# Performance work log

Measured on AMD Instinct MI355X. Metric: run time of the kernel, lower is better.

## Reference

```python
import jax, jax.numpy as jnp
import numpy as np

WORD, D, H = 512, 64, 8  # word_size, embed_dim (per-head), n_query

def setup_inputs() -> dict:
    key = jax.random.key(0)
    ks = jax.random.split(key, 9)
    B, S = 2, 4096
    sw = 1.0 / np.sqrt(WORD)
    x  = jax.random.normal(ks[0], (B, S, WORD), dtype=jnp.float32)
    Wk = jax.random.normal(ks[1], (WORD, D), dtype=jnp.float32) * sw
    bk = jnp.zeros((D,), jnp.float32)
    Wv = jax.random.normal(ks[2], (WORD, D), dtype=jnp.float32) * sw
    bv = jnp.zeros((D,), jnp.float32)
    Wq = jax.random.normal(ks[3], (H, WORD, D), dtype=jnp.float32) * sw
    bq = jnp.zeros((H, D), jnp.float32)
    Wp = jax.random.normal(ks[4], (H * D, D), dtype=jnp.float32) * (1.0 / np.sqrt(H * D))
    bp = jnp.zeros((D,), jnp.float32)
    return {"x": x, "Wq": Wq, "bq": bq, "Wk": Wk, "bk": bk, "Wv": Wv, "bv": bv, "Wp": Wp, "bp": bp}

def reference(x, Wq, bq, Wk, bk, Wv, bv, Wp, bp):
    # shared K/V across all query heads (multi-query attention)
    K = x @ Wk + bk                                   # [b, s, d]
    V = x @ Wv + bv                                   # [b, s, d]
    Q = jnp.einsum('bsw,hwd->bhsd', x, Wq) + bq[None, :, None, :]  # [b, h, s, d]
    scale = 1.0 / jnp.sqrt(jnp.float32(D))
    scores = jnp.einsum('bhsd,btd->bhst', Q, K) * scale  # [b, h, s, t]
    attn = jax.nn.softmax(scores, axis=-1)
    Z = jnp.einsum('bhst,btd->bhsd', attn, V)            # [b, h, s, d]
    B, _, S, _ = Z.shape
    Zc = jnp.transpose(Z, (0, 2, 1, 3)).reshape(B, S, H * D)  # concat heads
    return Zc @ Wp + bp                                   # [b, s, d]
```

## Files before the change

### kernel.cpp

```cpp
#include <hip/hip_runtime.h>
#include <hip/hip_bf16.h>
#include <stdint.h>

#define BB 2
#define SS 4096
#define WW 512
#define DD 64
#define HH 8
#define QSCALE 0.1803368801111244f

typedef __hip_bfloat16 bf16;
typedef __bf16 bf16x8 __attribute__((ext_vector_type(8)));
typedef float f32x16 __attribute__((ext_vector_type(16)));
typedef unsigned int u32x4 __attribute__((ext_vector_type(4)));
typedef unsigned int u32x2 __attribute__((ext_vector_type(2)));

union U4 { u32x4 u4; unsigned int u[4]; bf16x8 v; };

__device__ __forceinline__ float ldv(const float* p, size_t i) { return p[i]; }
__device__ __forceinline__ float ldv(const bf16* p, size_t i)  { return __bfloat162float(p[i]); }

__device__ __forceinline__ unsigned short f2bu(float f) {
    union Ub { bf16 b; unsigned short u; } t;
    t.b = __float2bfloat16(f);
    return t.u;
}

__device__ __forceinline__ float fast_exp2(float x) {
#if __has_builtin(__builtin_amdgcn_exp2f)
    return __builtin_amdgcn_exp2f(x);
#else
    return exp2f(x);
#endif
}

__device__ __forceinline__ f32x16 mfma_bf16(bf16x8 a, bf16x8 b, f32x16 c) {
    return __builtin_amdgcn_mfma_f32_32x32x16_bf16(a, b, c, 0, 0, 0);
}

__device__ __forceinline__ unsigned int pk_bf16(float lo, float hi) {
    unsigned int a = __float_as_uint(lo) + 0x8000u;
    unsigned int b = __float_as_uint(hi) + 0x8000u;
    return __builtin_amdgcn_perm(b, a, 0x07060302u);
}

__device__ __forceinline__ int block_detect(const void* raw, int* cntLds)
{
    if (threadIdx.x == 0) *cntLds = 0;
    __syncthreads();
    const bf16* xb = (const bf16*)raw;
    const float v = __bfloat162float(xb[2 * threadIdx.x]);
    const float a = fabsf(v);
    const bool insane = !(v == v) || (a >= 1.0e4f) || (a != 0.0f && a <= 1.0e-8f);
    const unsigned long long m = __ballot(insane);
    if ((threadIdx.x & 63) == 0) atomicAdd(cntLds, __popcll(m));
    __syncthreads();
    return (*cntLds * 2 > 256) ? 1 : 0;
}

template<typename T>
__device__ __forceinline__ void prep_w_body(
    const T* Wq, const T* bq, const T* Wk, const T* bk,
    const T* Wv, const T* bv, const T* Wp, const T* bp,
    unsigned short* Wb, float* bb, float (*Tt)[65], int pwblk)
{
    const int tid = threadIdx.x;
    const int cg = pwblk >> 3, wg = pwblk & 7;
    const int c0 = cg * 64, w0 = wg * 64;
    const T* src = (cg == 0) ? Wk : (cg == 1) ? Wv
                 : (cg == 10) ? Wp : (Wq + (size_t)(cg - 2) * WW * DD);
    const float scale = (cg >= 2 && cg < 10) ? QSCALE : 1.0f;

    #pragma unroll
    for (int i = 0; i < 16; ++i) {
        const int e = i * 256 + tid, w = e >> 6, d = e & 63;
        Tt[w][d] = ldv(src, (size_t)(w0 + w) * DD + d) * scale;
    }
    __syncthreads();
    #pragma unroll
    for (int i = 0; i < 16; ++i) {
        const int e = i * 256 + tid, d = e >> 6, w = e & 63;
        Wb[(size_t)(c0 + d) * WW + w0 + w] = f2bu(Tt[w][d]);
    }
    if (pwblk == 0) {
        #pragma unroll
        for (int i = 0; i < 3; ++i) {
            const int c = tid + i * 256;
            if (c < 704) {
                float v;
                if (c < 64)       v = ldv(bk, c);
                else if (c < 128) v = ldv(bv, c - 64);
                else if (c < 640) v = ldv(bq, c - 128) * QSCALE;
                else              v = ldv(bp, c - 640);
                bb[c] = v;
            }
        }
    }
}

__global__ __launch_bounds__(256) void prep_kernel(
    const void* x, const void* Wq, const void* bq, const void* Wk, const void* bk,
    const void* Wv, const void* bv, const void* Wp, const void* bp,
    unsigned short* xb, unsigned short* Wb, float* bb, int* flag)
{
    __shared__ float Tt[64][65];
    __shared__ int cnt;
    const int blk = blockIdx.x;

    if (blk < 2048) {
        const int fl = block_detect(x, &cnt);
        if (blk == 0 && threadIdx.x == 0) *flag = fl;
        const size_t i = ((size_t)blk * 256 + threadIdx.x) * 8;
        if (fl) {
            const float4* p = (const float4*)((const float*)x + i);
            const float4 a = p[0], b = p[1];
            unsigned int w[4];
            w[0] = pk_bf16(a.x, a.y); w[1] = pk_bf16(a.z, a.w);
            w[2] = pk_bf16(b.x, b.y); w[3] = pk_bf16(b.z, b.w);
            *(u32x4*)(xb + i) = *(u32x4*)w;
        } else {
            *(u32x4*)(xb + i) = *(const u32x4*)((const unsigned short*)x + i);
        }
    } else {
        const int fl = block_detect(Wk, &cnt);
        if (fl)
            prep_w_body<float>((const float*)Wq, (const float*)bq, (const float*)Wk,
                               (const float*)bk, (const float*)Wv, (const float*)bv,
                               (const float*)Wp, (const float*)bp, Wb, bb, Tt, blk - 2048);
        else
            prep_w_body<bf16>((const bf16*)Wq, (const bf16*)bq, (const bf16*)Wk,
                              (const bf16*)bk, (const bf16*)Wv, (const bf16*)bv,
                              (const bf16*)Wp, (const bf16*)bp, Wb, bb, Tt, blk - 2048);
    }
}

#define KP 40

__global__ __launch_bounds__(256, 2) void proj_mfma_kernel(
    const unsigned short* __restrict__ xb, const unsigned short* __restrict__ Wb,
    const float* __restrict__ bb,
    bf16* __restrict__ Kb, bf16* __restrict__ Vb, bf16* __restrict__ Qb)
{
    __shared__ unsigned short As[2][128 * KP];
    __shared__ unsigned short Bs[2][128 * KP];

    const int tid = threadIdx.x;
    const int wv = tid >> 6, ln = tid & 63;
    const int g = ln >> 5, cc = ln & 31;
    const int nblk = blockIdx.x % 5, mblk = blockIdx.x / 5;
    const int row0 = mblk * 128, n0 = nblk * 128;
    const int wm = (wv & 1) * 64, wn = (wv >> 1) * 64;

    const int sm = tid >> 2;
    const int sko = (tid & 3) * 8;

    u32x4 pa[2], pb[2];
    #define GLOAD(kt)                                                          \
        do {                                                                   \
            _Pragma("unroll")                                                  \
            for (int i = 0; i < 2; ++i) {                                      \
                const int m = sm + i * 64;                                     \
                pa[i] = *(const u32x4*)&xb[(size_t)(row0 + m) * WW + (kt) * 32 + sko]; \
                pb[i] = *(const u32x4*)&Wb[(size_t)(n0 + m) * WW + (kt) * 32 + sko];   \
            }                                                                  \
        } while (0)
    #define LWRITE(buf)                                                        \
        do {                                                                   \
            _Pragma("unroll")                                                  \
            for (int i = 0; i < 2; ++i) {                                      \
                const int m = sm + i * 64;                                     \
                *(u32x4*)&As[buf][m * KP + sko] = pa[i];                       \
                *(u32x4*)&Bs[buf][m * KP + sko] = pb[i];                       \
            }                                                                  \
        } while (0)

    f32x16 acc[2][2];
    #pragma unroll
    for (int a = 0; a < 2; ++a)
        #pragma unroll
        for (int c2 = 0; c2 < 2; ++c2)
            #pragma unroll
            for (int i = 0; i < 16; ++i) acc[a][c2][i] = 0.f;

    GLOAD(0); LWRITE(0);
    GLOAD(1);

    for (int kt = 0; kt < 16; ++kt) {
        __syncthreads();
        const int buf = kt & 1;
        #pragma unroll
        for (int ks = 0; ks < 2; ++ks) {
            U4 af[2], bfr[2];
            #pragma unroll
            for (int ms = 0; ms < 2; ++ms)
                af[ms].u4 = *(const u32x4*)&As[buf][(wm + ms * 32 + cc) * KP + ks * 16 + g * 8];
            #pragma unroll
            for (int ns = 0; ns < 2; ++ns)
                bfr[ns].u4 = *(const u32x4*)&Bs[buf][(wn + ns * 32 + cc) * KP + ks * 16 + g * 8];
            #pragma unroll
            for (int ms = 0; ms < 2; ++ms)
                #pragma unroll
                for (int ns = 0; ns < 2; ++ns)
                    acc[ms][ns] = mfma_bf16(af[ms].v, bfr[ns].v, acc[ms][ns]);
        }
        if (kt < 15) {
            LWRITE(buf ^ 1);
            if (kt < 14) GLOAD(kt + 2);
        }
    }
    #undef GLOAD
    #undef LWRITE

    const int b = row0 >> 12;
    #pragma unroll
    for (int ns = 0; ns < 2; ++ns) {
        const int c = n0 + wn + ns * 32 + cc;
        const int grp = c >> 6, d = c & 63;
        const float bias = bb[c];
        bf16* base = (grp == 0) ? Kb : (grp == 1) ? Vb
                   : Qb + (size_t)((b * HH + grp - 2) - b) * SS * DD;
        #pragma unroll
        for (int ms = 0; ms < 2; ++ms) {
            #pragma unroll
            for (int reg = 0; reg < 16; ++reg) {
                const int r = (reg & 3) + 8 * (reg >> 2) + 4 * g;
                const int row = row0 + wm + ms * 32 + r;
                base[(size_t)row * DD + d] = __float2bfloat16(acc[ms][ns][reg] + bias);
            }
        }
    }
}

__device__ __forceinline__ int vperm(int r) {
    return (r & ~31) + 16 * ((r >> 4) & 1) + 8 * ((r >> 2) & 1)
         + 4 * ((r >> 3) & 1) + (r & 3);
}

__global__ __launch_bounds__(256) void vtrans_kernel(
    const unsigned short* __restrict__ Vb, unsigned short* __restrict__ Vtg)
{
    __shared__ unsigned short Ls[64 * 70];
    const int tid = threadIdx.x;
    const int bb = blockIdx.x >> 6;
    const int t0 = (blockIdx.x & 63) * 64;
    const unsigned short* in = Vb + ((size_t)bb * SS + t0) * DD;

    const int lt = tid >> 2, s2 = tid & 3;
    #pragma unroll
    for (int q2 = 0; q2 < 2; ++q2) {
        const int sg = s2 + q2 * 4;
        *(u32x4*)&Ls[lt * 70 + sg * 8] = *(const u32x4*)&in[lt * 64 + sg * 8];
    }
    __syncthreads();

    const int dd = tid >> 2, t2 = tid & 3;
    unsigned short* op = Vtg + ((size_t)bb * DD + dd) * SS + t0;
    #pragma unroll
    for (int q2 = 0; q2 < 2; ++q2) {
        const int ts = (t2 + q2 * 4) * 8;
        unsigned short tmp[8];
        #pragma unroll
        for (int j = 0; j < 8; ++j) tmp[j] = Ls[(ts + j) * 70 + dd];
        const int s0 = vperm(ts);
        const int s1 = vperm(ts + 4);
        *(u32x2*)&op[s0] = *(u32x2*)&tmp[0];
        *(u32x2*)&op[s1] = *(u32x2*)&tmp[4];
    }
}

#define VTP 72
#define ZP_PART ((size_t)16 * 64 * 4096)
#define LP_PART ((size_t)16 * 4096)

template<int TSPLIT>
__global__ __launch_bounds__(256, 4) void attn_mfma_kernel(
    const bf16* __restrict__ Kb, const unsigned short* __restrict__ Vtg,
    const bf16* __restrict__ Qb, bf16* __restrict__ Zb,
    float* __restrict__ Zp, float* __restrict__ Lp)
{
    __shared__ unsigned short Vt[2][64 * VTP];
    __shared__ unsigned short Kt[2][64 * VTP];

    const int tid = threadIdx.x;
    const int wv = tid >> 6, ln = tid & 63;
    const int g  = ln >> 5, cc = ln & 31;
    const int chunk = blockIdx.x & 31;
    const int tsp = (TSPLIT == 1) ? 0 : ((blockIdx.x >> 5) & 1);
    const int bh  = blockIdx.x >> ((TSPLIT == 1) ? 5 : 6);
    const int b = bh >> 3, h = bh & 7;
    const int qw = chunk * 128 + wv * 32;
    const int it0 = tsp * (64 / TSPLIT);
    const int itN = it0 + 64 / TSPLIT;

    const unsigned short* Kg = (const unsigned short*)(Kb + (size_t)b * SS * DD);
    const unsigned short* Vg = Vtg + (size_t)b * DD * SS;
    const char* Qg = (const char*)(Qb + (size_t)(b * HH + h) * SS * DD);

    const int sr = tid >> 2, sc = (tid & 3) * 16;
    const unsigned short* VgRow = Vg + (size_t)sr * SS;

    U4 qf[4];
    #pragma unroll
    for (int ks = 0; ks < 4; ++ks)
        qf[ks].u4 = *(const u32x4*)(Qg +
            (size_t)((qw + cc) * 64 + g * 8 + ks * 16) * 2);

    f32x16 zacc[2];
    #pragma unroll
    for (int dt = 0; dt < 2; ++dt)
        #pragma unroll
        for (int i = 0; i < 16; ++i) zacc[dt][i] = 0.f;

    float la = 0.f, lb2 = 0.f;

    {
        const unsigned short* ksrc = Kg + (size_t)(it0 * 64 + sr) * 64 + sc;
        const unsigned short* vsrc = VgRow + it0 * 64 + sc;
        *(u32x4*)&Kt[0][sr * VTP + sc + 0] = *(const u32x4*)&ksrc[0];
        *(u32x4*)&Kt[0][sr * VTP + sc + 8] = *(const u32x4*)&ksrc[8];
        *(u32x4*)&Vt[0][sr * VTP + sc + 0] = *(const u32x4*)&vsrc[0];
        *(u32x4*)&Vt[0][sr * VTP + sc + 8] = *(const u32x4*)&vsrc[8];
    }

    for (int it = it0; it < itN; ++it) {
        __syncthreads();
        const int buf = it & 1;
        const bool more = (it + 1) < itN;
        u32x4 pk0, pk1, pv0, pv1;
        if (more) {
            const unsigned short* ksrc = Kg + (size_t)((it + 1) * 64 + sr) * 64 + sc;
            const unsigned short* vsrc = VgRow + (it + 1) * 64 + sc;
            pk0 = *(const u32x4*)&ksrc[0];
            pk1 = *(const u32x4*)&ksrc[8];
            pv0 = *(const u32x4*)&vsrc[0];
            pv1 = *(const u32x4*)&vsrc[8];
        }

        #pragma unroll
        for (int si = 0; si < 2; ++si) {
            U4 kf[4];
            #pragma unroll
            for (int ks = 0; ks < 4; ++ks)
                kf[ks].u4 = *(const u32x4*)&Kt[buf][(si * 32 + cc) * VTP +
                                                    ks * 16 + g * 8];

            f32x16 s;
            #pragma unroll
            for (int i = 0; i < 16; ++i) s[i] = 0.f;
            #pragma unroll
            for (int ks = 0; ks < 4; ++ks) s = mfma_bf16(kf[ks].v, qf[ks].v, s);

            float p[16];
            #pragma unroll
            for (int i = 0; i < 16; ++i) p[i] = fast_exp2(s[i]);
            #pragma unroll
            for (int i = 0; i < 8; ++i) { la += p[i]; lb2 += p[8 + i]; }

            unsigned int w0[8];
            #pragma unroll
            for (int i2 = 0; i2 < 8; ++i2)
                w0[i2] = pk_bf16(p[2 * i2], p[2 * i2 + 1]);

            #pragma unroll
            for (int ks = 0; ks < 2; ++ks) {
                U4 pb;
                pb.u[0] = w0[ks * 4 + 0]; pb.u[1] = w0[ks * 4 + 1];
                pb.u[2] = w0[ks * 4 + 2]; pb.u[3] = w0[ks * 4 + 3];
                #pragma unroll
                for (int dt = 0; dt < 2; ++dt) {
                    U4 vf;
                    vf.u4 = *(const u32x4*)&Vt[buf][(dt * 32 + cc) * VTP +
                                                    si * 32 + ks * 16 + g * 8];
                    zacc[dt] = mfma_bf16(vf.v, pb.v, zacc[dt]);
                }
            }
        }

        if (more) {
            *(u32x4*)&Kt[buf ^ 1][sr * VTP + sc + 0] = pk0;
            *(u32x4*)&Kt[buf ^ 1][sr * VTP + sc + 8] = pk1;
            *(u32x4*)&Vt[buf ^ 1][sr * VTP + sc + 0] = pv0;
            *(u32x4*)&Vt[buf ^ 1][sr * VTP + sc + 8] = pv1;
        }
    }

    float l = la + lb2;
    l += __shfl_xor(l, 32, 64);

    if (TSPLIT == 1) {
        const float rr = 1.0f / l;
        bf16* zp = Zb + (size_t)(b * SS + qw + cc) * (HH * DD) + h * DD + g * 4;
        #pragma unroll
        for (int dt = 0; dt < 2; ++dt)
            #pragma unroll
            for (int i = 0; i < 16; ++i) {
                const int d = (i & 3) + 8 * (i >> 2) + 32 * dt;
                zp[d] = __float2bfloat16(zacc[dt][i] * rr);
            }
    } else {
        float* zp0 = Zp + (size_t)(tsp * 16 + bh) * (64 * 4096);
        #pragma unroll
        for (int dt = 0; dt < 2; ++dt)
            #pragma unroll
            for (int i = 0; i < 16; ++i) {
                const int d = (i & 3) + 8 * (i >> 2) + 4 * g + 32 * dt;
                zp0[(size_t)d * 4096 + qw + cc] = zacc[dt][i];
            }
        if (g == 0)
            Lp[(size_t)(tsp * 16 + bh) * 4096 + qw + cc] = l;
    }
}

__global__ __launch_bounds__(256) void combine_kernel(
    const float* __restrict__ Zp, const float* __restrict__ Lp,
    bf16* __restrict__ Zb)
{
    const size_t T = (size_t)blockIdx.x * 256 + threadIdx.x;
    const int sblk = (int)(T & 511);
    const int d  = (int)((T >> 9) & 63);
    const int bh = (int)(T >> 15);
    const int s0 = sblk * 8;
    const int b = bh >> 3, h = bh & 7;

    const float* p0 = Zp + ((size_t)bh * 64 + d) * 4096 + s0;
    const float* p1 = p0 + ZP_PART;
    const float* l0 = Lp + (size_t)bh * 4096 + s0;
    const float* l1 = l0 + LP_PART;

    float z[8], lv[8];
    #pragma unroll
    for (int j = 0; j < 8; j += 4) {
        const float4 a = *(const float4*)(p0 + j);
        const float4 c = *(const float4*)(p1 + j);
        z[j] = a.x + c.x; z[j+1] = a.y + c.y; z[j+2] = a.z + c.z; z[j+3] = a.w + c.w;
        const float4 e = *(const float4*)(l0 + j);
        const float4 f = *(const float4*)(l1 + j);
        lv[j] = e.x + f.x; lv[j+1] = e.y + f.y; lv[j+2] = e.z + f.z; lv[j+3] = e.w + f.w;
    }
    bf16* zo = Zb + ((size_t)(b * SS + s0)) * (HH * DD) + h * DD + d;
    #pragma unroll
    for (int j = 0; j < 8; ++j)
        zo[(size_t)j * (HH * DD)] = __float2bfloat16(z[j] / lv[j]);
}

__global__ __launch_bounds__(256) void outp_mfma_kernel(
    const bf16* __restrict__ Zb, const unsigned short* __restrict__ Wb,
    const float* __restrict__ bb, const int* flag, void* out)
{
    __shared__ unsigned short As[2][128 * KP];
    __shared__ unsigned short Bs[2][64 * KP];

    const int tid = threadIdx.x;
    const int wv = tid >> 6, ln = tid & 63;
    const int g = ln >> 5, cc = ln & 31;
    const int row0 = blockIdx.x * 128;
    const int sm = tid >> 2, sko = (tid & 3) * 8;

    const unsigned short* Zu = (const unsigned short*)Zb;
    const unsigned short* Wn = Wb + (size_t)640 * WW;
    const float* bbp = bb + 640;

    u32x4 pa[2], pbv;
    #define GLOAD2(kt)                                                         \
        do {                                                                   \
            _Pragma("unroll")                                                  \
            for (int i = 0; i < 2; ++i)                                        \
                pa[i] = *(const u32x4*)&Zu[(size_t)(row0 + sm + i * 64) * WW + (kt) * 32 + sko]; \
            pbv = *(const u32x4*)&Wn[(size_t)sm * WW + (kt) * 32 + sko];       \
        } while (0)
    #define LWRITE2(buf)                                                       \
        do {                                                                   \
            _Pragma("unroll")                                                  \
            for (int i = 0; i < 2; ++i)                                        \
                *(u32x4*)&As[buf][(sm + i * 64) * KP + sko] = pa[i];           \
            *(u32x4*)&Bs[buf][sm * KP + sko] = pbv;                            \
        } while (0)

    f32x16 acc[2];
    #pragma unroll
    for (int ns = 0; ns < 2; ++ns)
        #pragma unroll
        for (int i = 0; i < 16; ++i) acc[ns][i] = 0.f;

    GLOAD2(0); LWRITE2(0);
    GLOAD2(1);

    for (int kt = 0; kt < 16; ++kt) {
        __syncthreads();
        const int buf = kt & 1;
        #pragma unroll
        for (int ks = 0; ks < 2; ++ks) {
            U4 af;
            af.u4 = *(const u32x4*)&As[buf][(wv * 32 + cc) * KP + ks * 16 + g * 8];
            #pragma unroll
            for (int ns = 0; ns < 2; ++ns) {
                U4 bf2;
                bf2.u4 = *(const u32x4*)&Bs[buf][(ns * 32 + cc) * KP + ks * 16 + g * 8];
                acc[ns] = mfma_bf16(af.v, bf2.v, acc[ns]);
            }
        }
        if (kt < 15) {
            LWRITE2(buf ^ 1);
            if (kt < 14) GLOAD2(kt + 2);
        }
    }
    #undef GLOAD2
    #undef LWRITE2

    const int fl = *flag;
    #pragma unroll
    for (int ns = 0; ns < 2; ++ns) {
        const int c = ns * 32 + cc;
        const float bias = bbp[c];
        #pragma unroll
        for (int reg = 0; reg < 16; ++reg) {
            const int r = (reg & 3) + 8 * (reg >> 2) + 4 * g;
            const int row = row0 + wv * 32 + r;
            const float v = acc[ns][reg] + bias;
            if (fl) ((float*)out)[(size_t)row * DD + c] = v;
            else    ((bf16*)out)[(size_t)row * DD + c] = __float2bfloat16(v);
        }
    }
}

extern "C" void kernel_launch(void* const* d_in, const int* in_sizes, int n_in,
                              void* d_out, int out_size, void* d_ws, size_t ws_size,
                              hipStream_t stream)
{
    const void* x  = d_in[0];
    const void* Wq = d_in[1];
    const void* bq = d_in[2];
    const void* Wk = d_in[3];
    const void* bk = d_in[4];
    const void* Wv = d_in[5];
    const void* bv = d_in[6];
    const void* Wp = d_in[7];
    const void* bp = d_in[8];

    char* ws = (char*)d_ws;
    bf16* Kb = (bf16*)(ws);
    bf16* Vb = (bf16*)(ws + (1u << 20));
    bf16* Qb = (bf16*)(ws + (2u << 20));
    bf16* Zb = (bf16*)(ws + (10u << 20));
    unsigned short* xb = (unsigned short*)(ws + (10u << 20));
    int* flag = (int*)(ws + (18u << 20));
    unsigned short* Wb = (unsigned short*)(ws + (18u << 20) + 64);
    float* bb = (float*)(ws + (18u << 20) + 64 + 704 * 512 * 2);
    unsigned short* Vtg = (unsigned short*)(ws + (19u << 20));
    float* Zp = (float*)(ws + (20u << 20));
    float* Lp = (float*)(ws + (20u << 20) + 2 * ZP_PART * 4);

    const size_t ws_need_split = (20u << 20) + 2 * ZP_PART * 4 + 2 * LP_PART * 4;
    const bool split = ws_size >= ws_need_split;

    prep_kernel<<<2136, 256, 0, stream>>>(x, Wq, bq, Wk, bk, Wv, bv, Wp, bp,
                                          xb, Wb, bb, flag);
    proj_mfma_kernel<<<320, 256, 0, stream>>>(xb, Wb, bb, Kb, Vb, Qb);
    vtrans_kernel<<<128, 256, 0, stream>>>((const unsigned short*)Vb, Vtg);
    if (split) {
        attn_mfma_kernel<2><<<1024, 256, 0, stream>>>(Kb, Vtg, Qb, Zb, Zp, Lp);
        combine_kernel<<<2048, 256, 0, stream>>>(Zp, Lp, Zb);
    } else {
        attn_mfma_kernel<1><<<512, 256, 0, stream>>>(Kb, Vtg, Qb, Zb, Zp, Lp);
    }
    outp_mfma_kernel<<<64, 256, 0, stream>>>(Zb, Wb, bb, flag, d_out);
}
```

Baseline: 206.9 us.

## Load K/V MFMA fragments directly from global memory, dropping LDS staging

The attention kernel no longer stages K and V tiles through double-buffered shared memory with a block-wide barrier each iteration. Each wave now loads its K and V MFMA operand fragments straight from global memory (via cache) and register-prefetches the next K fragment. This removes the LDS traffic and __syncthreads, but each of the four waves now fetches the same K/V data on its own, relying on L1/L2 hits, and V loads are not prefetched ahead of use.

```diff
diff --git a/kernel.cpp b/kernel.cpp
--- a/kernel.cpp
+++ b/kernel.cpp
@@ -268,7 +268,6 @@
     }
 }
 
-#define VTP 72
 #define ZP_PART ((size_t)16 * 64 * 4096)
 #define LP_PART ((size_t)16 * 4096)
 
@@ -278,9 +277,6 @@
     const bf16* __restrict__ Qb, bf16* __restrict__ Zb,
     float* __restrict__ Zp, float* __restrict__ Lp)
 {
-    __shared__ unsigned short Vt[2][64 * VTP];
-    __shared__ unsigned short Kt[2][64 * VTP];
-
     const int tid = threadIdx.x;
     const int wv = tid >> 6, ln = tid & 63;
     const int g  = ln >> 5, cc = ln & 31;
@@ -296,9 +292,6 @@
     const unsigned short* Vg = Vtg + (size_t)b * DD * SS;
     const char* Qg = (const char*)(Qb + (size_t)(b * HH + h) * SS * DD);
 
-    const int sr = tid >> 2, sc = (tid & 3) * 16;
-    const unsigned short* VgRow = Vg + (size_t)sr * SS;
-
     U4 qf[4];
     #pragma unroll
     for (int ks = 0; ks < 4; ++ks)
@@ -313,36 +306,39 @@
 
     float la = 0.f, lb2 = 0.f;
 
+    const unsigned short* kbase  = Kg + (size_t)cc * 64 + g * 8;
+    const unsigned short* v0base = Vg + (size_t)cc * SS + g * 8;
+    const unsigned short* v1base = v0base + (size_t)32 * SS;
+
+    U4 kfn[4];
     {
-        const unsigned short* ksrc = Kg + (size_t)(it0 * 64 + sr) * 64 + sc;
-        const unsigned short* vsrc = VgRow + it0 * 64 + sc;
-        *(u32x4*)&Kt[0][sr * VTP + sc + 0] = *(const u32x4*)&ksrc[0];
-        *(u32x4*)&Kt[0][sr * VTP + sc + 8] = *(const u32x4*)&ksrc[8];
-        *(u32x4*)&Vt[0][sr * VTP + sc + 0] = *(const u32x4*)&vsrc[0];
-        *(u32x4*)&Vt[0][sr * VTP + sc + 8] = *(const u32x4*)&vsrc[8];
+        const unsigned short* kp = kbase + (size_t)(it0 * 64) * 64;
+        #pragma unroll
+        for (int ks = 0; ks < 4; ++ks) kfn[ks].u4 = *(const u32x4*)(kp + ks * 16);
     }
 
     for (int it = it0; it < itN; ++it) {
-        __syncthreads();
-        const int buf = it & 1;
-        const bool more = (it + 1) < itN;
-        u32x4 pk0, pk1, pv0, pv1;
-        if (more) {
-            const unsigned short* ksrc = Kg + (size_t)((it + 1) * 64 + sr) * 64 + sc;
-            const unsigned short* vsrc = VgRow + (it + 1) * 64 + sc;
-            pk0 = *(const u32x4*)&ksrc[0];
-            pk1 = *(const u32x4*)&ksrc[8];
-            pv0 = *(const u32x4*)&vsrc[0];
-            pv1 = *(const u32x4*)&vsrc[8];
-        }
-
+        const int t0 = it * 64;
         #pragma unroll
         for (int si = 0; si < 2; ++si) {
+            const int tt = t0 + si * 32;
+
+            U4 vf[2][2];
+            #pragma unroll
+            for (int ks = 0; ks < 2; ++ks) {
+                vf[ks][0].u4 = *(const u32x4*)(v0base + tt + ks * 16);
+                vf[ks][1].u4 = *(const u32x4*)(v1base + tt + ks * 16);
+            }
+
             U4 kf[4];
             #pragma unroll
-            for (int ks = 0; ks < 4; ++ks)
-                kf[ks].u4 = *(const u32x4*)&Kt[buf][(si * 32 + cc) * VTP +
-                                                    ks * 16 + g * 8];
+            for (int ks = 0; ks < 4; ++ks) kf[ks] = kfn[ks];
+            const int tn = tt + 32;
+            if (tn < itN * 64) {
+                const unsigned short* kp = kbase + (size_t)tn * 64;
+                #pragma unroll
+                for (int ks = 0; ks < 4; ++ks) kfn[ks].u4 = *(const u32x4*)(kp + ks * 16);
+            }
 
             f32x16 s;
             #pragma unroll
@@ -367,20 +363,9 @@
                 pb.u[0] = w0[ks * 4 + 0]; pb.u[1] = w0[ks * 4 + 1];
                 pb.u[2] = w0[ks * 4 + 2]; pb.u[3] = w0[ks * 4 + 3];
                 #pragma unroll
-                for (int dt = 0; dt < 2; ++dt) {
-                    U4 vf;
-                    vf.u4 = *(const u32x4*)&Vt[buf][(dt * 32 + cc) * VTP +
-                                                    si * 32 + ks * 16 + g * 8];
-                    zacc[dt] = mfma_bf16(vf.v, pb.v, zacc[dt]);
-                }
-            }
-        }
-
-        if (more) {
-            *(u32x4*)&Kt[buf ^ 1][sr * VTP + sc + 0] = pk0;
-            *(u32x4*)&Kt[buf ^ 1][sr * VTP + sc + 8] = pk1;
-            *(u32x4*)&Vt[buf ^ 1][sr * VTP + sc + 0] = pv0;
-            *(u32x4*)&Vt[buf ^ 1][sr * VTP + sc + 8] = pv1;
+                for (int dt = 0; dt < 2; ++dt)
+                    zacc[dt] = mfma_bf16(vf[ks][dt].v, pb.v, zacc[dt]);
+            }
         }
     }
 
```

Result: slower. 394.8 us (+90.8%).

## Process two query tiles per wave to reuse K/V fragments in attention

Applied to the files above, without the earlier changes.

Each wave now handles 64 query rows (two 32-row tiles) instead of 32, so every K and V fragment read from shared memory feeds twice as many MFMAs. The grid is halved and the launch bound is lowered to 2 blocks per CU to allow more registers for the doubled accumulators and Q fragments. This cuts LDS traffic and global K/V loads per query, at the cost of higher register pressure, lower occupancy, and fewer blocks, which hurts latency hiding and load balance across CUs.

```diff
diff --git a/kernel.cpp b/kernel.cpp
--- a/kernel.cpp
+++ b/kernel.cpp
@@ -273,7 +273,7 @@
 #define LP_PART ((size_t)16 * 4096)
 
 template<int TSPLIT>
-__global__ __launch_bounds__(256, 4) void attn_mfma_kernel(
+__global__ __launch_bounds__(256, 2) void attn_mfma_kernel(
     const bf16* __restrict__ Kb, const unsigned short* __restrict__ Vtg,
     const bf16* __restrict__ Qb, bf16* __restrict__ Zb,
     float* __restrict__ Zp, float* __restrict__ Lp)
@@ -284,11 +284,11 @@
     const int tid = threadIdx.x;
     const int wv = tid >> 6, ln = tid & 63;
     const int g  = ln >> 5, cc = ln & 31;
-    const int chunk = blockIdx.x & 31;
-    const int tsp = (TSPLIT == 1) ? 0 : ((blockIdx.x >> 5) & 1);
-    const int bh  = blockIdx.x >> ((TSPLIT == 1) ? 5 : 6);
+    const int chunk = blockIdx.x & 15;
+    const int tsp = (TSPLIT == 1) ? 0 : ((blockIdx.x >> 4) & 1);
+    const int bh  = blockIdx.x >> ((TSPLIT == 1) ? 4 : 5);
     const int b = bh >> 3, h = bh & 7;
-    const int qw = chunk * 128 + wv * 32;
+    const int qw = chunk * 256 + wv * 64;
     const int it0 = tsp * (64 / TSPLIT);
     const int itN = it0 + 64 / TSPLIT;
 
@@ -299,19 +299,23 @@
     const int sr = tid >> 2, sc = (tid & 3) * 16;
     const unsigned short* VgRow = Vg + (size_t)sr * SS;
 
-    U4 qf[4];
-    #pragma unroll
-    for (int ks = 0; ks < 4; ++ks)
-        qf[ks].u4 = *(const u32x4*)(Qg +
-            (size_t)((qw + cc) * 64 + g * 8 + ks * 16) * 2);
-
-    f32x16 zacc[2];
-    #pragma unroll
-    for (int dt = 0; dt < 2; ++dt)
-        #pragma unroll
-        for (int i = 0; i < 16; ++i) zacc[dt][i] = 0.f;
-
-    float la = 0.f, lb2 = 0.f;
+    U4 qf[2][4];
+    #pragma unroll
+    for (int nt = 0; nt < 2; ++nt)
+        #pragma unroll
+        for (int ks = 0; ks < 4; ++ks)
+            qf[nt][ks].u4 = *(const u32x4*)(Qg +
+                (size_t)((qw + nt * 32 + cc) * 64 + g * 8 + ks * 16) * 2);
+
+    f32x16 zacc[2][2];
+    #pragma unroll
+    for (int nt = 0; nt < 2; ++nt)
+        #pragma unroll
+        for (int dt = 0; dt < 2; ++dt)
+            #pragma unroll
+            for (int i = 0; i < 16; ++i) zacc[nt][dt][i] = 0.f;
+
+    float la0 = 0.f, lb0 = 0.f, la1 = 0.f, lb1 = 0.f;
 
     {
         const unsigned short* ksrc = Kg + (size_t)(it0 * 64 + sr) * 64 + sc;
@@ -343,35 +347,46 @@
             for (int ks = 0; ks < 4; ++ks)
                 kf[ks].u4 = *(const u32x4*)&Kt[buf][(si * 32 + cc) * VTP +
                                                     ks * 16 + g * 8];
-
-            f32x16 s;
-            #pragma unroll
-            for (int i = 0; i < 16; ++i) s[i] = 0.f;
-            #pragma unroll
-            for (int ks = 0; ks < 4; ++ks) s = mfma_bf16(kf[ks].v, qf[ks].v, s);
-
-            float p[16];
-            #pragma unroll
-            for (int i = 0; i < 16; ++i) p[i] = fast_exp2(s[i]);
-            #pragma unroll
-            for (int i = 0; i < 8; ++i) { la += p[i]; lb2 += p[8 + i]; }
-
-            unsigned int w0[8];
-            #pragma unroll
-            for (int i2 = 0; i2 < 8; ++i2)
-                w0[i2] = pk_bf16(p[2 * i2], p[2 * i2 + 1]);
-
-            #pragma unroll
-            for (int ks = 0; ks < 2; ++ks) {
-                U4 pb;
-                pb.u[0] = w0[ks * 4 + 0]; pb.u[1] = w0[ks * 4 + 1];
-                pb.u[2] = w0[ks * 4 + 2]; pb.u[3] = w0[ks * 4 + 3];
-                #pragma unroll
-                for (int dt = 0; dt < 2; ++dt) {
-                    U4 vf;
-                    vf.u4 = *(const u32x4*)&Vt[buf][(dt * 32 + cc) * VTP +
-                                                    si * 32 + ks * 16 + g * 8];
-                    zacc[dt] = mfma_bf16(vf.v, pb.v, zacc[dt]);
+            U4 vf[2][2];
+            #pragma unroll
+            for (int ks = 0; ks < 2; ++ks)
+                #pragma unroll
+                for (int dt = 0; dt < 2; ++dt)
+                    vf[ks][dt].u4 = *(const u32x4*)&Vt[buf][(dt * 32 + cc) * VTP +
+                                                            si * 32 + ks * 16 + g * 8];
+
+            #pragma unroll
+            for (int nt = 0; nt < 2; ++nt) {
+                f32x16 s;
+                #pragma unroll
+                for (int i = 0; i < 16; ++i) s[i] = 0.f;
+                #pragma unroll
+                for (int ks = 0; ks < 4; ++ks) s = mfma_bf16(kf[ks].v, qf[nt][ks].v, s);
+
+                float p[16];
+                #pragma unroll
+                for (int i = 0; i < 16; ++i) p[i] = fast_exp2(s[i]);
+                if (nt == 0) {
+                    #pragma unroll
+                    for (int i = 0; i < 8; ++i) { la0 += p[i]; lb0 += p[8 + i]; }
+                } else {
+                    #pragma unroll
+                    for (int i = 0; i < 8; ++i) { la1 += p[i]; lb1 += p[8 + i]; }
+                }
+
+                unsigned int w0[8];
+                #pragma unroll
+                for (int i2 = 0; i2 < 8; ++i2)
+                    w0[i2] = pk_bf16(p[2 * i2], p[2 * i2 + 1]);
+
+                #pragma unroll
+                for (int ks = 0; ks < 2; ++ks) {
+                    U4 pb;
+                    pb.u[0] = w0[ks * 4 + 0]; pb.u[1] = w0[ks * 4 + 1];
+                    pb.u[2] = w0[ks * 4 + 2]; pb.u[3] = w0[ks * 4 + 3];
+                    #pragma unroll
+                    for (int dt = 0; dt < 2; ++dt)
+                        zacc[nt][dt] = mfma_bf16(vf[ks][dt].v, pb.v, zacc[nt][dt]);
                 }
             }
         }
@@ -384,30 +399,42 @@
         }
     }
 
-    float l = la + lb2;
-    l += __shfl_xor(l, 32, 64);
+    float l[2];
+    l[0] = la0 + lb0;
+    l[1] = la1 + lb1;
+    #pragma unroll
+    for (int nt = 0; nt < 2; ++nt)
+        l[nt] += __shfl_xor(l[nt], 32, 64);
 
     if (TSPLIT == 1) {
-        const float rr = 1.0f / l;
-        bf16* zp = Zb + (size_t)(b * SS + qw + cc) * (HH * DD) + h * DD + g * 4;
-        #pragma unroll
-        for (int dt = 0; dt < 2; ++dt)
-            #pragma unroll
-            for (int i = 0; i < 16; ++i) {
-                const int d = (i & 3) + 8 * (i >> 2) + 32 * dt;
-                zp[d] = __float2bfloat16(zacc[dt][i] * rr);
-            }
+        #pragma unroll
+        for (int nt = 0; nt < 2; ++nt) {
+            const float rr = 1.0f / l[nt];
+            bf16* zp = Zb + (size_t)(b * SS + qw + nt * 32 + cc) * (HH * DD)
+                     + h * DD + g * 4;
+            #pragma unroll
+            for (int dt = 0; dt < 2; ++dt)
+                #pragma unroll
+                for (int i = 0; i < 16; ++i) {
+                    const int d = (i & 3) + 8 * (i >> 2) + 32 * dt;
+                    zp[d] = __float2bfloat16(zacc[nt][dt][i] * rr);
+                }
+        }
     } else {
         float* zp0 = Zp + (size_t)(tsp * 16 + bh) * (64 * 4096);
         #pragma unroll
-        for (int dt = 0; dt < 2; ++dt)
-            #pragma unroll
-            for (int i = 0; i < 16; ++i) {
-                const int d = (i & 3) + 8 * (i >> 2) + 4 * g + 32 * dt;
-                zp0[(size_t)d * 4096 + qw + cc] = zacc[dt][i];
-            }
-        if (g == 0)
-            Lp[(size_t)(tsp * 16 + bh) * 4096 + qw + cc] = l;
+        for (int nt = 0; nt < 2; ++nt) {
+            const int q = qw + nt * 32 + cc;
+            #pragma unroll
+            for (int dt = 0; dt < 2; ++dt)
+                #pragma unroll
+                for (int i = 0; i < 16; ++i) {
+                    const int d = (i & 3) + 8 * (i >> 2) + 4 * g + 32 * dt;
+                    zp0[(size_t)d * 4096 + q] = zacc[nt][dt][i];
+                }
+            if (g == 0)
+                Lp[(size_t)(tsp * 16 + bh) * 4096 + q] = l[nt];
+        }
     }
 }
 
@@ -558,10 +585,10 @@
     proj_mfma_kernel<<<320, 256, 0, stream>>>(xb, Wb, bb, Kb, Vb, Qb);
     vtrans_kernel<<<128, 256, 0, stream>>>((const unsigned short*)Vb, Vtg);
     if (split) {
-        attn_mfma_kernel<2><<<1024, 256, 0, stream>>>(Kb, Vtg, Qb, Zb, Zp, Lp);
+        attn_mfma_kernel<2><<<512, 256, 0, stream>>>(Kb, Vtg, Qb, Zb, Zp, Lp);
         combine_kernel<<<2048, 256, 0, stream>>>(Zp, Lp, Zb);
     } else {
-        attn_mfma_kernel<1><<<512, 256, 0, stream>>>(Kb, Vtg, Qb, Zb, Zp, Lp);
+        attn_mfma_kernel<1><<<256, 256, 0, stream>>>(Kb, Vtg, Qb, Zb, Zp, Lp);
     }
     outp_mfma_kernel<<<64, 256, 0, stream>>>(Zb, Wb, bb, flag, d_out);
 }
```

New measurement: 198.9 us. -3.9%, faster.
